# Kernel optimization log

Hardware: AMD Instinct MI355X
Metric: run time of the kernel (lower is better)

The kernel has to match this reference:

```python
import jax, jax.numpy as jnp
import numpy as np

B, T, XD, ZD, H = 1024, 1000, 8, 8, 256


def setup_inputs() -> dict:
    key = jax.random.key(0)
    ks = jax.random.split(key, 10)
    # monotonically increasing time grid, identical per batch element: [B, T, 1]
    t = jnp.broadcast_to(jnp.linspace(0.0, 10.0, T, dtype=jnp.float32)[None, :, None], (B, T, 1))
    x = jax.random.normal(ks[0], (B, T, XD), jnp.float32)
    z = jax.random.normal(ks[1], (B, T, ZD), jnp.float32)
    event_t = jax.random.uniform(ks[2], (B, 1), jnp.float32, 3.0, 7.0)
    z_jump = jax.random.normal(ks[3], (B, ZD), jnp.float32)
    in_dim = 3 * (XD + ZD)

    def lin(k, fan_in, fan_out):
        return jax.random.normal(k, (fan_in, fan_out), jnp.float32) * (1.0 / np.sqrt(fan_in))

    W1 = lin(ks[4], in_dim, H); b1 = jnp.zeros((H,), jnp.float32)
    W2 = lin(ks[5], H, H);     b2 = jnp.zeros((H,), jnp.float32)
    W3 = lin(ks[6], H, H);     b3 = jnp.zeros((H,), jnp.float32)
    W4 = lin(ks[7], H, XD);    b4 = jnp.zeros((XD,), jnp.float32)
    return dict(t=t, x=x, z=z, event_t=event_t, z_jump=z_jump,
                W1=W1, b1=b1, W2=W2, b2=b2, W3=W3, b3=b3, W4=W4, b4=b4)


def reference(t, x, z, event_t, z_jump, W1, b1, W2, b2, W3, b3, W4, b4):
    # all_initial = cat(x[:,0], z[:,0]) : [B, XD+ZD]
    all_initial = jnp.concatenate([x[:, 0], z[:, 0]], axis=-1)

    def de_func(x_cur, z_eff):
        xtzt = jnp.concatenate([x_cur, z_eff], axis=-1)                      # [B, XD+ZD]
        inp = jnp.concatenate([all_initial, xtzt - all_initial, xtzt], -1)   # [B, 3*(XD+ZD)]
        h = jax.nn.elu(inp @ W1 + b1)
        h = jax.nn.elu(h @ W2 + b2)
        h = jax.nn.elu(h @ W3 + b3)
        return h @ W4 + b4                                                   # [B, XD]

    t_seq = jnp.moveaxis(t, 1, 0)   # [T, B, 1]
    z_seq = jnp.moveaxis(z, 1, 0)   # [T, B, ZD]
    dt = t_seq[1:] - t_seq[:-1]     # [T-1, B, 1]

    def step(x_cur, step_in):
        t_i, dt_i, z_i = step_in
        # event: once t passes event_t, exogenous z jumps to z_jump
        z_eff = jnp.where(t_i >= event_t, z_jump, z_i)
        x_next = x_cur + dt_i * de_func(x_cur, z_eff)  # explicit Euler step
        return x_next, x_next

    x0 = x[:, 0]  # initial condition [B, XD]
    _, xs = jax.lax.scan(step, x0, (t_seq[:-1], dt, z_seq[:-1]))
    sol = jnp.concatenate([x0[None], xs], axis=0)  # [T, B, XD]
    return jnp.moveaxis(sol, 0, 1)                 # [B, T, XD]
```

## Files before the change

kernel.cpp:

```cpp
#include <hip/hip_runtime.h>
#include <cstdint>
#include <cstddef>

typedef __bf16 bf16x8 __attribute__((ext_vector_type(8)));
typedef float f32x4 __attribute__((ext_vector_type(4)));

#define HD 256
#define TLEN 1000
#define NSTEP 999
#define BTILE 4

#define W1R_OFF 0
#define W2R_OFF 16384
#define W3R_OFF 81920
#define W4R_OFF 147456
#define WS_ELEMS 151552

__device__ __forceinline__ void wg_barrier() {
  asm volatile("s_waitcnt lgkmcnt(0)\n\ts_barrier" ::: "memory");
}

__global__ void prep_weights(const float* __restrict__ W1, const float* __restrict__ b1,
                             const float* __restrict__ W2, const float* __restrict__ W3,
                             const float* __restrict__ W4, __bf16* __restrict__ ws) {
  int tid = blockIdx.x * blockDim.x + threadIdx.x;
  if (tid >= WS_ELEMS) return;
  float val = 0.0f;
  if (tid < W2R_OFF) {
    int t = tid;
    int j = t & 7, lane = (t >> 3) & 63, tt = (t >> 9) & 1, kb = (t >> 10) & 1, w = (t >> 11) & 7;
    int k = kb * 32 + ((lane >> 4) * 8) + j;
    int n = w * 32 + tt * 16 + (lane & 15);
    if (k < 48) val = W1[k * HD + n];
    else if (k == 48) val = b1[n];
  } else if (tid < W3R_OFF) {
    int t = tid - W2R_OFF;
    int j = t & 7, lane = (t >> 3) & 63, tt = (t >> 9) & 1, kb = (t >> 10) & 7, w = (t >> 13) & 7;
    int k = kb * 32 + ((lane >> 4) * 8) + j;
    int n = w * 32 + tt * 16 + (lane & 15);
    val = W2[k * HD + n];
  } else if (tid < W4R_OFF) {
    int t = tid - W3R_OFF;
    int j = t & 7, lane = (t >> 3) & 63, tt = (t >> 9) & 1, kb = (t >> 10) & 7, w = (t >> 13) & 7;
    int k = kb * 32 + ((lane >> 4) * 8) + j;
    int n = w * 32 + tt * 16 + (lane & 15);
    val = W3[k * HD + n];
  } else {
    int t = tid - W4R_OFF;
    int j = t & 7, lane = (t >> 3) & 63, kb = (t >> 9) & 7;
    int k = kb * 32 + ((lane >> 4) * 8) + j;
    int n = lane & 15;
    val = (n < 8) ? W4[k * 8 + n] : 0.0f;
  }
  ws[tid] = (__bf16)val;
}

__global__ __launch_bounds__(512, 2) void ode_main(
    const float* __restrict__ t_g, const float* __restrict__ x_g,
    const float* __restrict__ z_g, const float* __restrict__ ev_g,
    const float* __restrict__ zj_g, const float* __restrict__ b2_g,
    const float* __restrict__ b3_g, const float* __restrict__ b4_g,
    const __bf16* __restrict__ ws, float* __restrict__ out) {
  __shared__ __align__(16) __bf16 h_a[16 * 264];
  __shared__ __align__(16) __bf16 h_b[16 * 264];
  __shared__ __align__(16) float p4[8 * 16 * 8];
  __shared__ __align__(16) float x_cur[16 * 12];
  __shared__ __align__(16) float z_eff[16 * 12];
  __shared__ __align__(16) float x0s[16 * 12];
  __shared__ __align__(16) float z0s[16 * 12];
  __shared__ __align__(16) float zjs[16 * 12];
  __shared__ float evs[16];

  const int tid  = threadIdx.x;
  const int lane = tid & 63;
  const int wid  = tid >> 6;
  const int bcol = lane & 15;
  const int q    = lane >> 4;
  const int b0   = blockIdx.x * BTILE;
  const bool live = bcol < BTILE;

  if (tid < 128) {
    int m = tid >> 3, d = tid & 7;
    if (m < BTILE) {
      size_t gb = (size_t)(b0 + m);
      float x0 = x_g[gb * (TLEN * 8) + d];
      float z0 = z_g[gb * (TLEN * 8) + d];
      x0s[m * 12 + d] = x0;
      z0s[m * 12 + d] = z0;
      x_cur[m * 12 + d] = x0;
      zjs[m * 12 + d] = zj_g[gb * 8 + d];
      out[gb * (TLEN * 8) + d] = x0;
      if (d == 0) evs[m] = ev_g[gb];
    } else {
      x0s[m * 12 + d] = 0.f;
      z0s[m * 12 + d] = 0.f;
      x_cur[m * 12 + d] = 0.f;
      zjs[m * 12 + d] = 0.f;
      if (d == 0) evs[m] = 0.f;
    }
  }
  __syncthreads();

  if (tid < 128) {
    int m = tid >> 3, d = tid & 7;
    float t0 = t_g[0];
    z_eff[m * 12 + d] = (t0 >= evs[m]) ? zjs[m * 12 + d] : z0s[m * 12 + d];
  }

  const bf16x8* wsv = (const bf16x8*)ws;
  bf16x8 w1f[2][2], w2f[8][2], w3f[8][2];
#pragma unroll
  for (int kb = 0; kb < 2; ++kb)
#pragma unroll
    for (int tt = 0; tt < 2; ++tt)
      w1f[kb][tt] = wsv[(W1R_OFF / 8) + ((wid * 2 + kb) * 2 + tt) * 64 + lane];
#pragma unroll
  for (int kb = 0; kb < 8; ++kb)
#pragma unroll
    for (int tt = 0; tt < 2; ++tt) {
      w2f[kb][tt] = wsv[(W2R_OFF / 8) + ((wid * 8 + kb) * 2 + tt) * 64 + lane];
      w3f[kb][tt] = wsv[(W3R_OFF / 8) + ((wid * 8 + kb) * 2 + tt) * 64 + lane];
    }
  bf16x8 w4f = wsv[(W4R_OFF / 8) + wid * 64 + lane];

  f32x4 b2v[2], b3v[2];
#pragma unroll
  for (int tt = 0; tt < 2; ++tt) {
    int n0 = wid * 32 + tt * 16 + q * 4;
    b2v[tt] = *(const f32x4*)(b2_g + n0);
    b3v[tt] = *(const f32x4*)(b3_g + n0);
  }
  float b4l = (tid < 64) ? b4_g[tid & 7] : 0.0f;

  const int m1 = lane >> 2;
  const int d0 = (lane & 3) * 2;
  float2 zjf = make_float2(0.f, 0.f);
  float ev1 = 0.f;
  const bool zprod = (wid == 2) && (lane < BTILE * 4);
  if (zprod) {
    zjf.x = zjs[m1 * 12 + d0];
    zjf.y = zjs[m1 * 12 + d0 + 1];
    ev1 = evs[m1];
  }

  f32x4 sub0, sub1;
  bf16x8 a0c;
  {
    const float* base = ((q & 1) ? z0s : x0s) + bcol * 12;
    f32x4 r0 = *(const f32x4*)(base);
    f32x4 r1 = *(const f32x4*)(base + 4);
    sub0 = r0; sub1 = r1;
#pragma unroll
    for (int e = 0; e < 4; ++e) { a0c[e] = (__bf16)r0[e]; a0c[e + 4] = (__bf16)r1[e]; }
  }
  bf16x8 zf;
#pragma unroll
  for (int e = 0; e < 8; ++e) zf[e] = (__bf16)0.f;
  bf16x8 k48f = zf;
  k48f[0] = (__bf16)1.0f;

  __syncthreads();

  float tc = t_g[0];

  bf16x8 bfr[8];
#pragma unroll
  for (int kb = 0; kb < 8; ++kb) bfr[kb] = zf;
  bf16x8 h4r = zf;

  auto layer = [&](const __bf16* src, __bf16* dst, const bf16x8 (*wf)[2], const f32x4* bv) {
    const bf16x8* hp = (const bf16x8*)src;
    if (live) {
#pragma unroll
      for (int kb = 0; kb < 8; ++kb) bfr[kb] = hp[bcol * 33 + kb * 4 + q];
    }
#pragma unroll
    for (int tt = 0; tt < 2; ++tt) {
      f32x4 c = bv[tt];
#pragma unroll
      for (int kb = 0; kb < 8; ++kb)
        c = __builtin_amdgcn_mfma_f32_16x16x32_bf16(wf[kb][tt], bfr[kb], c, 0, 0, 0);
      union { __bf16 h4[4]; unsigned long long u; } pk;
#pragma unroll
      for (int e = 0; e < 4; ++e) {
        float v = c[e];
        v = (v > 0.f) ? v : (__expf(v) - 1.0f);
        pk.h4[e] = (__bf16)v;
      }
      if (live)
        *(unsigned long long*)(dst + bcol * 264 + wid * 32 + tt * 16 + q * 4) = pk.u;
    }
  };

#pragma unroll 1
  for (int i = 0; i < NSTEP; ++i) {
    float tn = t_g[i + 1];
    float2 zpre = make_float2(0.f, 0.f);
    if (zprod)
      zpre = *(const float2*)(z_g + ((size_t)(b0 + m1) * TLEN + (i + 1)) * 8 + d0);

    {
      const float* rp = ((q & 1) ? z_eff : x_cur) + bcol * 12;
      f32x4 r0 = *(const f32x4*)(rp);
      f32x4 r1 = *(const f32x4*)(rp + 4);
      bf16x8 f0, f1;
      if (q < 2) {
        f0 = a0c;
#pragma unroll
        for (int e = 0; e < 4; ++e) { f1[e] = (__bf16)r0[e]; f1[e + 4] = (__bf16)r1[e]; }
      } else {
#pragma unroll
        for (int e = 0; e < 4; ++e) {
          f0[e] = (__bf16)(r0[e] - sub0[e]);
          f0[e + 4] = (__bf16)(r1[e] - sub1[e]);
        }
        f1 = (q == 2) ? k48f : zf;
      }
#pragma unroll
      for (int tt = 0; tt < 2; ++tt) {
        f32x4 c = {0.f, 0.f, 0.f, 0.f};
        c = __builtin_amdgcn_mfma_f32_16x16x32_bf16(w1f[0][tt], f0, c, 0, 0, 0);
        c = __builtin_amdgcn_mfma_f32_16x16x32_bf16(w1f[1][tt], f1, c, 0, 0, 0);
        union { __bf16 h4[4]; unsigned long long u; } pk;
#pragma unroll
        for (int e = 0; e < 4; ++e) {
          float v = c[e];
          v = (v > 0.f) ? v : (__expf(v) - 1.0f);
          pk.h4[e] = (__bf16)v;
        }
        if (live)
          *(unsigned long long*)(h_a + bcol * 264 + wid * 32 + tt * 16 + q * 4) = pk.u;
      }
    }
    wg_barrier();
    layer(h_a, h_b, w2f, b2v);
    wg_barrier();
    layer(h_b, h_a, w3f, b3v);

    {
      const bf16x8* hp = (const bf16x8*)h_a;
      if (live) h4r = hp[bcol * 33 + wid * 4 + q];
      f32x4 c = {0.f, 0.f, 0.f, 0.f};
      c = __builtin_amdgcn_mfma_f32_16x16x32_bf16(w4f, h4r, c, 0, 0, 0);
      if (q < 2 && live)
        *(f32x4*)(p4 + wid * 128 + bcol * 8 + q * 4) = c;
    }
    wg_barrier();

    float dt = tn - tc;
    if (tid < 64) {
      int m = tid >> 3, d = tid & 7;
      if (m < BTILE) {
        float s = b4l;
#pragma unroll
        for (int j = 0; j < 8; ++j) s += p4[j * 128 + m * 8 + d];
        float xn = x_cur[m * 12 + d] + dt * s;
        x_cur[m * 12 + d] = xn;
        out[(size_t)(b0 + m) * (TLEN * 8) + (size_t)(i + 1) * 8 + d] = xn;
      }
    } else if (zprod) {
      bool jmp = (tn >= ev1);
      float2 zev = make_float2(jmp ? zjf.x : zpre.x, jmp ? zjf.y : zpre.y);
      *(float2*)(z_eff + m1 * 12 + d0) = zev;
    }
    tc = tn;
    wg_barrier();
  }
}

extern "C" void kernel_launch(void* const* d_in, const int* in_sizes, int n_in,
                              void* d_out, int out_size, void* d_ws, size_t ws_size,
                              hipStream_t stream) {
  const float* t  = (const float*)d_in[0];
  const float* x  = (const float*)d_in[1];
  const float* z  = (const float*)d_in[2];
  const float* ev = (const float*)d_in[3];
  const float* zj = (const float*)d_in[4];
  const float* W1 = (const float*)d_in[5];
  const float* b1 = (const float*)d_in[6];
  const float* W2 = (const float*)d_in[7];
  const float* b2 = (const float*)d_in[8];
  const float* W3 = (const float*)d_in[9];
  const float* b3 = (const float*)d_in[10];
  const float* W4 = (const float*)d_in[11];
  const float* b4 = (const float*)d_in[12];
  __bf16* ws = (__bf16*)d_ws;
  float* out = (float*)d_out;

  prep_weights<<<592, 256, 0, stream>>>(W1, b1, W2, W3, W4, ws);
  ode_main<<<256, 512, 0, stream>>>(t, x, z, ev, zj, b2, b3, b4, ws, out);
}
```

Baseline: 1.671 ms.

## Compute layer-4 redundantly in every wave to drop the partial-sum reduction barrier

Previously each wave computed a slice of the final HxXD product, wrote partials to shared memory, synchronized, and a single wave reduced them and updated x. Now layer 3 writes to a third buffer, and every wave loads the full hidden vector and runs all 8 K-blocks of the output MFMA. Each wave then updates x in registers itself. This replaces the partial-sum barrier with one placed before layer 4, and keeps the state in registers. The cost is redundant MFMA work, more weight registers per wave (w4f grows to 8 fragments), and racy identical writes to x_cur and z_eff from all waves.

```diff
diff --git a/kernel.cpp b/kernel.cpp
--- a/kernel.cpp
+++ b/kernel.cpp
@@ -63,7 +63,7 @@
     const __bf16* __restrict__ ws, float* __restrict__ out) {
   __shared__ __align__(16) __bf16 h_a[16 * 264];
   __shared__ __align__(16) __bf16 h_b[16 * 264];
-  __shared__ __align__(16) float p4[8 * 16 * 8];
+  __shared__ __align__(16) __bf16 h_c[16 * 264];
   __shared__ __align__(16) float x_cur[16 * 12];
   __shared__ __align__(16) float z_eff[16 * 12];
   __shared__ __align__(16) float x0s[16 * 12];
@@ -78,19 +78,20 @@
   const int q    = lane >> 4;
   const int b0   = blockIdx.x * BTILE;
   const bool live = bcol < BTILE;
+  const size_t gb = (size_t)(b0 + (live ? bcol : 0));
 
   if (tid < 128) {
     int m = tid >> 3, d = tid & 7;
     if (m < BTILE) {
-      size_t gb = (size_t)(b0 + m);
-      float x0 = x_g[gb * (TLEN * 8) + d];
-      float z0 = z_g[gb * (TLEN * 8) + d];
+      size_t g = (size_t)(b0 + m);
+      float x0 = x_g[g * (TLEN * 8) + d];
+      float z0 = z_g[g * (TLEN * 8) + d];
       x0s[m * 12 + d] = x0;
       z0s[m * 12 + d] = z0;
       x_cur[m * 12 + d] = x0;
-      zjs[m * 12 + d] = zj_g[gb * 8 + d];
-      out[gb * (TLEN * 8) + d] = x0;
-      if (d == 0) evs[m] = ev_g[gb];
+      zjs[m * 12 + d] = zj_g[g * 8 + d];
+      out[g * (TLEN * 8) + d] = x0;
+      if (d == 0) evs[m] = ev_g[g];
     } else {
       x0s[m * 12 + d] = 0.f;
       z0s[m * 12 + d] = 0.f;
@@ -108,20 +109,21 @@
   }
 
   const bf16x8* wsv = (const bf16x8*)ws;
-  bf16x8 w1f[2][2], w2f[8][2], w3f[8][2];
+  bf16x8 w1f[2][2], w2f[8][2], w3f[8][2], w4f[8];
 #pragma unroll
   for (int kb = 0; kb < 2; ++kb)
 #pragma unroll
     for (int tt = 0; tt < 2; ++tt)
       w1f[kb][tt] = wsv[(W1R_OFF / 8) + ((wid * 2 + kb) * 2 + tt) * 64 + lane];
 #pragma unroll
-  for (int kb = 0; kb < 8; ++kb)
+  for (int kb = 0; kb < 8; ++kb) {
 #pragma unroll
     for (int tt = 0; tt < 2; ++tt) {
       w2f[kb][tt] = wsv[(W2R_OFF / 8) + ((wid * 8 + kb) * 2 + tt) * 64 + lane];
       w3f[kb][tt] = wsv[(W3R_OFF / 8) + ((wid * 8 + kb) * 2 + tt) * 64 + lane];
     }
-  bf16x8 w4f = wsv[(W4R_OFF / 8) + wid * 64 + lane];
+    w4f[kb] = wsv[(W4R_OFF / 8) + kb * 64 + lane];
+  }
 
   f32x4 b2v[2], b3v[2];
 #pragma unroll
@@ -130,14 +132,15 @@
     b2v[tt] = *(const f32x4*)(b2_g + n0);
     b3v[tt] = *(const f32x4*)(b3_g + n0);
   }
-  float b4l = (tid < 64) ? b4_g[tid & 7] : 0.0f;
+  f32x4 b4v = {0.f, 0.f, 0.f, 0.f};
+  if (q < 2) b4v = *(const f32x4*)(b4_g + q * 4);
 
   const int m1 = lane >> 2;
   const int d0 = (lane & 3) * 2;
+  const bool zp = (lane < 16);
   float2 zjf = make_float2(0.f, 0.f);
   float ev1 = 0.f;
-  const bool zprod = (wid == 2) && (lane < BTILE * 4);
-  if (zprod) {
+  if (zp) {
     zjf.x = zjs[m1 * 12 + d0];
     zjf.y = zjs[m1 * 12 + d0 + 1];
     ev1 = evs[m1];
@@ -159,6 +162,9 @@
   bf16x8 k48f = zf;
   k48f[0] = (__bf16)1.0f;
 
+  f32x4 xc4 = {0.f, 0.f, 0.f, 0.f};
+  if (q < 2) xc4 = *(const f32x4*)(x0s + bcol * 12 + q * 4);
+
   __syncthreads();
 
   float tc = t_g[0];
@@ -166,7 +172,6 @@
   bf16x8 bfr[8];
 #pragma unroll
   for (int kb = 0; kb < 8; ++kb) bfr[kb] = zf;
-  bf16x8 h4r = zf;
 
   auto layer = [&](const __bf16* src, __bf16* dst, const bf16x8 (*wf)[2], const f32x4* bv) {
     const bf16x8* hp = (const bf16x8*)src;
@@ -196,7 +201,7 @@
   for (int i = 0; i < NSTEP; ++i) {
     float tn = t_g[i + 1];
     float2 zpre = make_float2(0.f, 0.f);
-    if (zprod)
+    if (zp)
       zpre = *(const float2*)(z_g + ((size_t)(b0 + m1) * TLEN + (i + 1)) * 8 + d0);
 
     {
@@ -235,36 +240,41 @@
     wg_barrier();
     layer(h_a, h_b, w2f, b2v);
     wg_barrier();
-    layer(h_b, h_a, w3f, b3v);
+    layer(h_b, h_c, w3f, b3v);
+    wg_barrier();
 
     {
-      const bf16x8* hp = (const bf16x8*)h_a;
-      if (live) h4r = hp[bcol * 33 + wid * 4 + q];
-      f32x4 c = {0.f, 0.f, 0.f, 0.f};
-      c = __builtin_amdgcn_mfma_f32_16x16x32_bf16(w4f, h4r, c, 0, 0, 0);
-      if (q < 2 && live)
-        *(f32x4*)(p4 + wid * 128 + bcol * 8 + q * 4) = c;
-    }
-    wg_barrier();
-
-    float dt = tn - tc;
-    if (tid < 64) {
-      int m = tid >> 3, d = tid & 7;
-      if (m < BTILE) {
-        float s = b4l;
-#pragma unroll
-        for (int j = 0; j < 8; ++j) s += p4[j * 128 + m * 8 + d];
-        float xn = x_cur[m * 12 + d] + dt * s;
-        x_cur[m * 12 + d] = xn;
-        out[(size_t)(b0 + m) * (TLEN * 8) + (size_t)(i + 1) * 8 + d] = xn;
-      }
-    } else if (zprod) {
-      bool jmp = (tn >= ev1);
-      float2 zev = make_float2(jmp ? zjf.x : zpre.x, jmp ? zjf.y : zpre.y);
-      *(float2*)(z_eff + m1 * 12 + d0) = zev;
+      const bf16x8* hp = (const bf16x8*)h_c;
+      if (live) {
+#pragma unroll
+        for (int kb = 0; kb < 8; ++kb) bfr[kb] = hp[bcol * 33 + kb * 4 + q];
+      }
+      f32x4 c0 = {0.f, 0.f, 0.f, 0.f}, c1 = {0.f, 0.f, 0.f, 0.f};
+#pragma unroll
+      for (int kb = 0; kb < 4; ++kb)
+        c0 = __builtin_amdgcn_mfma_f32_16x16x32_bf16(w4f[kb], bfr[kb], c0, 0, 0, 0);
+#pragma unroll
+      for (int kb = 4; kb < 8; ++kb)
+        c1 = __builtin_amdgcn_mfma_f32_16x16x32_bf16(w4f[kb], bfr[kb], c1, 0, 0, 0);
+      float dt = tn - tc;
+      if (q < 2) {
+        f32x4 xn;
+#pragma unroll
+        for (int e = 0; e < 4; ++e) xn[e] = xc4[e] + dt * (c0[e] + c1[e] + b4v[e]);
+        xc4 = xn;
+        if (live) {
+          *(f32x4*)(x_cur + bcol * 12 + q * 4) = xn;
+          if (wid == 0)
+            *(f32x4*)(out + gb * (TLEN * 8) + (size_t)(i + 1) * 8 + q * 4) = xn;
+        }
+      }
+      if (zp) {
+        bool jmp = (tn >= ev1);
+        float2 zev = make_float2(jmp ? zjf.x : zpre.x, jmp ? zjf.y : zpre.y);
+        *(float2*)(z_eff + m1 * 12 + d0) = zev;
+      }
     }
     tc = tn;
-    wg_barrier();
   }
 }
 
```

Result: slower. 2.786 ms (+66.8%).

## Split each MLP layer across 16 waves, one 16-column tile per wave

Applied to the files above, without the earlier changes.

Doubles the workgroup to 1024 threads so each wave owns a single 16-wide output tile instead of two, halving per-wave MFMA chains and the weight registers each wave holds. Layers 2 and 3 now use two independent accumulators to shorten the dependent MFMA chain. The W4 partial products are split across wave pairs, and the final reduction sums 16 partials. The cost is more waves contending at each barrier and a longer final reduction, and 1024-thread blocks may limit residency per CU.

```diff
diff --git a/kernel.cpp b/kernel.cpp
--- a/kernel.cpp
+++ b/kernel.cpp
@@ -55,7 +55,7 @@
   ws[tid] = (__bf16)val;
 }
 
-__global__ __launch_bounds__(512, 2) void ode_main(
+__global__ __launch_bounds__(1024, 4) void ode_main(
     const float* __restrict__ t_g, const float* __restrict__ x_g,
     const float* __restrict__ z_g, const float* __restrict__ ev_g,
     const float* __restrict__ zj_g, const float* __restrict__ b2_g,
@@ -63,7 +63,7 @@
     const __bf16* __restrict__ ws, float* __restrict__ out) {
   __shared__ __align__(16) __bf16 h_a[16 * 264];
   __shared__ __align__(16) __bf16 h_b[16 * 264];
-  __shared__ __align__(16) float p4[8 * 16 * 8];
+  __shared__ __align__(16) float p4[16 * 128];
   __shared__ __align__(16) float x_cur[16 * 12];
   __shared__ __align__(16) float z_eff[16 * 12];
   __shared__ __align__(16) float x0s[16 * 12];
@@ -74,7 +74,10 @@
   const int tid  = threadIdx.x;
   const int lane = tid & 63;
   const int wid  = tid >> 6;
+  const int pw   = wid >> 1;
+  const int ptt  = wid & 1;
   const int bcol = lane & 15;
+  const int rdcol= bcol & 3;
   const int q    = lane >> 4;
   const int b0   = blockIdx.x * BTILE;
   const bool live = bcol < BTILE;
@@ -82,15 +85,15 @@
   if (tid < 128) {
     int m = tid >> 3, d = tid & 7;
     if (m < BTILE) {
-      size_t gb = (size_t)(b0 + m);
-      float x0 = x_g[gb * (TLEN * 8) + d];
-      float z0 = z_g[gb * (TLEN * 8) + d];
+      size_t g = (size_t)(b0 + m);
+      float x0 = x_g[g * (TLEN * 8) + d];
+      float z0 = z_g[g * (TLEN * 8) + d];
       x0s[m * 12 + d] = x0;
       z0s[m * 12 + d] = z0;
       x_cur[m * 12 + d] = x0;
-      zjs[m * 12 + d] = zj_g[gb * 8 + d];
-      out[gb * (TLEN * 8) + d] = x0;
-      if (d == 0) evs[m] = ev_g[gb];
+      zjs[m * 12 + d] = zj_g[g * 8 + d];
+      out[g * (TLEN * 8) + d] = x0;
+      if (d == 0) evs[m] = ev_g[g];
     } else {
       x0s[m * 12 + d] = 0.f;
       z0s[m * 12 + d] = 0.f;
@@ -108,28 +111,19 @@
   }
 
   const bf16x8* wsv = (const bf16x8*)ws;
-  bf16x8 w1f[2][2], w2f[8][2], w3f[8][2];
+  bf16x8 w1f[2], w2f[8], w3f[8];
 #pragma unroll
   for (int kb = 0; kb < 2; ++kb)
-#pragma unroll
-    for (int tt = 0; tt < 2; ++tt)
-      w1f[kb][tt] = wsv[(W1R_OFF / 8) + ((wid * 2 + kb) * 2 + tt) * 64 + lane];
-#pragma unroll
-  for (int kb = 0; kb < 8; ++kb)
-#pragma unroll
-    for (int tt = 0; tt < 2; ++tt) {
-      w2f[kb][tt] = wsv[(W2R_OFF / 8) + ((wid * 8 + kb) * 2 + tt) * 64 + lane];
-      w3f[kb][tt] = wsv[(W3R_OFF / 8) + ((wid * 8 + kb) * 2 + tt) * 64 + lane];
-    }
-  bf16x8 w4f = wsv[(W4R_OFF / 8) + wid * 64 + lane];
-
-  f32x4 b2v[2], b3v[2];
-#pragma unroll
-  for (int tt = 0; tt < 2; ++tt) {
-    int n0 = wid * 32 + tt * 16 + q * 4;
-    b2v[tt] = *(const f32x4*)(b2_g + n0);
-    b3v[tt] = *(const f32x4*)(b3_g + n0);
-  }
+    w1f[kb] = wsv[(W1R_OFF / 8) + ((pw * 2 + kb) * 2 + ptt) * 64 + lane];
+#pragma unroll
+  for (int kb = 0; kb < 8; ++kb) {
+    w2f[kb] = wsv[(W2R_OFF / 8) + ((pw * 8 + kb) * 2 + ptt) * 64 + lane];
+    w3f[kb] = wsv[(W3R_OFF / 8) + ((pw * 8 + kb) * 2 + ptt) * 64 + lane];
+  }
+  bf16x8 w4f = wsv[(W4R_OFF / 8) + pw * 64 + lane];
+
+  f32x4 b2v = *(const f32x4*)(b2_g + wid * 16 + q * 4);
+  f32x4 b3v = *(const f32x4*)(b3_g + wid * 16 + q * 4);
   float b4l = (tid < 64) ? b4_g[tid & 7] : 0.0f;
 
   const int m1 = lane >> 2;
@@ -143,43 +137,78 @@
     ev1 = evs[m1];
   }
 
-  f32x4 sub0, sub1;
-  bf16x8 a0c;
-  {
-    const float* base = ((q & 1) ? z0s : x0s) + bcol * 12;
-    f32x4 r0 = *(const f32x4*)(base);
-    f32x4 r1 = *(const f32x4*)(base + 4);
-    sub0 = r0; sub1 = r1;
-#pragma unroll
-    for (int e = 0; e < 4; ++e) { a0c[e] = (__bf16)r0[e]; a0c[e + 4] = (__bf16)r1[e]; }
-  }
   bf16x8 zf;
 #pragma unroll
   for (int e = 0; e < 8; ++e) zf[e] = (__bf16)0.f;
-  bf16x8 k48f = zf;
-  k48f[0] = (__bf16)1.0f;
 
   __syncthreads();
 
   float tc = t_g[0];
 
-  bf16x8 bfr[8];
-#pragma unroll
-  for (int kb = 0; kb < 8; ++kb) bfr[kb] = zf;
-  bf16x8 h4r = zf;
-
-  auto layer = [&](const __bf16* src, __bf16* dst, const bf16x8 (*wf)[2], const f32x4* bv) {
+  auto layer = [&](const __bf16* src, __bf16* dst, const bf16x8* wf, f32x4 bv) {
     const bf16x8* hp = (const bf16x8*)src;
-    if (live) {
-#pragma unroll
-      for (int kb = 0; kb < 8; ++kb) bfr[kb] = hp[bcol * 33 + kb * 4 + q];
-    }
-#pragma unroll
-    for (int tt = 0; tt < 2; ++tt) {
-      f32x4 c = bv[tt];
-#pragma unroll
-      for (int kb = 0; kb < 8; ++kb)
-        c = __builtin_amdgcn_mfma_f32_16x16x32_bf16(wf[kb][tt], bfr[kb], c, 0, 0, 0);
+    bf16x8 f0 = hp[rdcol * 33 + 0 * 4 + q];
+    bf16x8 f1 = hp[rdcol * 33 + 1 * 4 + q];
+    bf16x8 f2 = hp[rdcol * 33 + 2 * 4 + q];
+    bf16x8 f3 = hp[rdcol * 33 + 3 * 4 + q];
+    bf16x8 f4 = hp[rdcol * 33 + 4 * 4 + q];
+    bf16x8 f5 = hp[rdcol * 33 + 5 * 4 + q];
+    bf16x8 f6 = hp[rdcol * 33 + 6 * 4 + q];
+    bf16x8 f7 = hp[rdcol * 33 + 7 * 4 + q];
+    f32x4 c0 = bv;
+    f32x4 c1 = {0.f, 0.f, 0.f, 0.f};
+    c0 = __builtin_amdgcn_mfma_f32_16x16x32_bf16(wf[0], f0, c0, 0, 0, 0);
+    c1 = __builtin_amdgcn_mfma_f32_16x16x32_bf16(wf[4], f4, c1, 0, 0, 0);
+    c0 = __builtin_amdgcn_mfma_f32_16x16x32_bf16(wf[1], f1, c0, 0, 0, 0);
+    c1 = __builtin_amdgcn_mfma_f32_16x16x32_bf16(wf[5], f5, c1, 0, 0, 0);
+    c0 = __builtin_amdgcn_mfma_f32_16x16x32_bf16(wf[2], f2, c0, 0, 0, 0);
+    c1 = __builtin_amdgcn_mfma_f32_16x16x32_bf16(wf[6], f6, c1, 0, 0, 0);
+    c0 = __builtin_amdgcn_mfma_f32_16x16x32_bf16(wf[3], f3, c0, 0, 0, 0);
+    c1 = __builtin_amdgcn_mfma_f32_16x16x32_bf16(wf[7], f7, c1, 0, 0, 0);
+    union { __bf16 h4[4]; unsigned long long u; } pk;
+#pragma unroll
+    for (int e = 0; e < 4; ++e) {
+      float v = c0[e] + c1[e];
+      v = (v > 0.f) ? v : (__expf(v) - 1.0f);
+      pk.h4[e] = (__bf16)v;
+    }
+    if (live)
+      *(unsigned long long*)(dst + bcol * 264 + wid * 16 + q * 4) = pk.u;
+  };
+
+#pragma unroll 1
+  for (int i = 0; i < NSTEP; ++i) {
+    float tn = t_g[i + 1];
+    float2 zpre = make_float2(0.f, 0.f);
+    if (zprod)
+      zpre = *(const float2*)(z_g + ((size_t)(b0 + m1) * TLEN + (i + 1)) * 8 + d0);
+
+    {
+      const float* rp = ((q & 1) ? z_eff : x_cur) + bcol * 12;
+      const float* sp = ((q & 1) ? z0s   : x0s  ) + bcol * 12;
+      f32x4 r0 = *(const f32x4*)(rp);
+      f32x4 r1 = *(const f32x4*)(rp + 4);
+      f32x4 s0 = *(const f32x4*)(sp);
+      f32x4 s1 = *(const f32x4*)(sp + 4);
+      bf16x8 f0, f1;
+      if (q < 2) {
+#pragma unroll
+        for (int e = 0; e < 4; ++e) {
+          f0[e] = (__bf16)s0[e]; f0[e + 4] = (__bf16)s1[e];
+          f1[e] = (__bf16)r0[e]; f1[e + 4] = (__bf16)r1[e];
+        }
+      } else {
+#pragma unroll
+        for (int e = 0; e < 4; ++e) {
+          f0[e] = (__bf16)(r0[e] - s0[e]);
+          f0[e + 4] = (__bf16)(r1[e] - s1[e]);
+        }
+        f1 = zf;
+        if (q == 2) f1[0] = (__bf16)1.0f;
+      }
+      f32x4 c = {0.f, 0.f, 0.f, 0.f};
+      c = __builtin_amdgcn_mfma_f32_16x16x32_bf16(w1f[0], f0, c, 0, 0, 0);
+      c = __builtin_amdgcn_mfma_f32_16x16x32_bf16(w1f[1], f1, c, 0, 0, 0);
       union { __bf16 h4[4]; unsigned long long u; } pk;
 #pragma unroll
       for (int e = 0; e < 4; ++e) {
@@ -188,60 +217,19 @@
         pk.h4[e] = (__bf16)v;
       }
       if (live)
-        *(unsigned long long*)(dst + bcol * 264 + wid * 32 + tt * 16 + q * 4) = pk.u;
-    }
-  };
-
-#pragma unroll 1
-  for (int i = 0; i < NSTEP; ++i) {
-    float tn = t_g[i + 1];
-    float2 zpre = make_float2(0.f, 0.f);
-    if (zprod)
-      zpre = *(const float2*)(z_g + ((size_t)(b0 + m1) * TLEN + (i + 1)) * 8 + d0);
+        *(unsigned long long*)(h_a + bcol * 264 + wid * 16 + q * 4) = pk.u;
+    }
+    wg_barrier();
+    layer(h_a, h_b, w2f, b2v);
+    wg_barrier();
+    layer(h_b, h_a, w3f, b3v);
 
     {
-      const float* rp = ((q & 1) ? z_eff : x_cur) + bcol * 12;
-      f32x4 r0 = *(const f32x4*)(rp);
-      f32x4 r1 = *(const f32x4*)(rp + 4);
-      bf16x8 f0, f1;
-      if (q < 2) {
-        f0 = a0c;
-#pragma unroll
-        for (int e = 0; e < 4; ++e) { f1[e] = (__bf16)r0[e]; f1[e + 4] = (__bf16)r1[e]; }
-      } else {
-#pragma unroll
-        for (int e = 0; e < 4; ++e) {
-          f0[e] = (__bf16)(r0[e] - sub0[e]);
-          f0[e + 4] = (__bf16)(r1[e] - sub1[e]);
-        }
-        f1 = (q == 2) ? k48f : zf;
-      }
-#pragma unroll
-      for (int tt = 0; tt < 2; ++tt) {
-        f32x4 c = {0.f, 0.f, 0.f, 0.f};
-        c = __builtin_amdgcn_mfma_f32_16x16x32_bf16(w1f[0][tt], f0, c, 0, 0, 0);
-        c = __builtin_amdgcn_mfma_f32_16x16x32_bf16(w1f[1][tt], f1, c, 0, 0, 0);
-        union { __bf16 h4[4]; unsigned long long u; } pk;
-#pragma unroll
-        for (int e = 0; e < 4; ++e) {
-          float v = c[e];
-          v = (v > 0.f) ? v : (__expf(v) - 1.0f);
-          pk.h4[e] = (__bf16)v;
-        }
-        if (live)
-          *(unsigned long long*)(h_a + bcol * 264 + wid * 32 + tt * 16 + q * 4) = pk.u;
-      }
-    }
-    wg_barrier();
-    layer(h_a, h_b, w2f, b2v);
-    wg_barrier();
-    layer(h_b, h_a, w3f, b3v);
-
-    {
-      const bf16x8* hp = (const bf16x8*)h_a;
-      if (live) h4r = hp[bcol * 33 + wid * 4 + q];
+      bf16x8 h4 = zf;
+      if (live && ((q >> 1) == ptt))
+        h4 = ((const bf16x8*)h_a)[bcol * 33 + pw * 4 + q];
       f32x4 c = {0.f, 0.f, 0.f, 0.f};
-      c = __builtin_amdgcn_mfma_f32_16x16x32_bf16(w4f, h4r, c, 0, 0, 0);
+      c = __builtin_amdgcn_mfma_f32_16x16x32_bf16(w4f, h4, c, 0, 0, 0);
       if (q < 2 && live)
         *(f32x4*)(p4 + wid * 128 + bcol * 8 + q * 4) = c;
     }
@@ -253,7 +241,7 @@
       if (m < BTILE) {
         float s = b4l;
 #pragma unroll
-        for (int j = 0; j < 8; ++j) s += p4[j * 128 + m * 8 + d];
+        for (int j = 0; j < 16; ++j) s += p4[j * 128 + m * 8 + d];
         float xn = x_cur[m * 12 + d] + dt * s;
         x_cur[m * 12 + d] = xn;
         out[(size_t)(b0 + m) * (TLEN * 8) + (size_t)(i + 1) * 8 + d] = xn;
@@ -288,5 +276,5 @@
   float* out = (float*)d_out;
 
   prep_weights<<<592, 256, 0, stream>>>(W1, b1, W2, W3, W4, ws);
-  ode_main<<<256, 512, 0, stream>>>(t, x, z, ev, zj, b2, b3, b4, ws, out);
-}
+  ode_main<<<256, 1024, 0, stream>>>(t, x, z, ev, zj, b2, b3, b4, ws, out);
+}
```

New measurement: 2.252 ms. 34.8% more time.

## Keep Euler state in registers and drop a per-step barrier

Applied to the files above, without the earlier changes.

Each wave now keeps the ODE state x and the effective z in registers. Every wave redundantly reduces the layer-4 partials from LDS and applies the Euler update, with wave shuffles assembling the layer-1 input. This removes the dedicated update phase and one workgroup barrier per time step, and the z and t loads for the next step are issued early. It also splits the layer-2/3 MFMA accumulation into two independent chains to shorten dependency latency, at the cost of redundant reduction work in every wave and a slightly different floating-point summation order.

```diff
diff --git a/kernel.cpp b/kernel.cpp
--- a/kernel.cpp
+++ b/kernel.cpp
@@ -63,13 +63,9 @@
     const __bf16* __restrict__ ws, float* __restrict__ out) {
   __shared__ __align__(16) __bf16 h_a[16 * 264];
   __shared__ __align__(16) __bf16 h_b[16 * 264];
-  __shared__ __align__(16) float p4[8 * 16 * 8];
-  __shared__ __align__(16) float x_cur[16 * 12];
-  __shared__ __align__(16) float z_eff[16 * 12];
+  __shared__ __align__(16) float p4[8 * 128];
   __shared__ __align__(16) float x0s[16 * 12];
   __shared__ __align__(16) float z0s[16 * 12];
-  __shared__ __align__(16) float zjs[16 * 12];
-  __shared__ float evs[16];
 
   const int tid  = threadIdx.x;
   const int lane = tid & 63;
@@ -78,34 +74,21 @@
   const int q    = lane >> 4;
   const int b0   = blockIdx.x * BTILE;
   const bool live = bcol < BTILE;
-
-  if (tid < 128) {
-    int m = tid >> 3, d = tid & 7;
-    if (m < BTILE) {
-      size_t gb = (size_t)(b0 + m);
-      float x0 = x_g[gb * (TLEN * 8) + d];
-      float z0 = z_g[gb * (TLEN * 8) + d];
-      x0s[m * 12 + d] = x0;
-      z0s[m * 12 + d] = z0;
-      x_cur[m * 12 + d] = x0;
-      zjs[m * 12 + d] = zj_g[gb * 8 + d];
-      out[gb * (TLEN * 8) + d] = x0;
-      if (d == 0) evs[m] = ev_g[gb];
-    } else {
-      x0s[m * 12 + d] = 0.f;
-      z0s[m * 12 + d] = 0.f;
-      x_cur[m * 12 + d] = 0.f;
-      zjs[m * 12 + d] = 0.f;
-      if (d == 0) evs[m] = 0.f;
-    }
-  }
+  const size_t gb = (size_t)(b0 + (live ? bcol : 0));
+
+  if (tid < 192) {
+    int m = tid / 12, d = tid % 12;
+    float xv = 0.f, zv = 0.f;
+    if (m < BTILE && d < 8) {
+      size_t g = (size_t)(b0 + m);
+      xv = x_g[g * (TLEN * 8) + d];
+      zv = z_g[g * (TLEN * 8) + d];
+    }
+    x0s[m * 12 + d] = xv;
+    z0s[m * 12 + d] = zv;
+  }
+  if (tid < 512) { p4[tid] = 0.f; if (tid < 512) { int t2 = tid + 512; if (t2 < 1024) p4[t2] = 0.f; } }
   __syncthreads();
-
-  if (tid < 128) {
-    int m = tid >> 3, d = tid & 7;
-    float t0 = t_g[0];
-    z_eff[m * 12 + d] = (t0 >= evs[m]) ? zjs[m * 12 + d] : z0s[m * 12 + d];
-  }
 
   const bf16x8* wsv = (const bf16x8*)ws;
   bf16x8 w1f[2][2], w2f[8][2], w3f[8][2];
@@ -130,18 +113,8 @@
     b2v[tt] = *(const f32x4*)(b2_g + n0);
     b3v[tt] = *(const f32x4*)(b3_g + n0);
   }
-  float b4l = (tid < 64) ? b4_g[tid & 7] : 0.0f;
-
-  const int m1 = lane >> 2;
-  const int d0 = (lane & 3) * 2;
-  float2 zjf = make_float2(0.f, 0.f);
-  float ev1 = 0.f;
-  const bool zprod = (wid == 2) && (lane < BTILE * 4);
-  if (zprod) {
-    zjf.x = zjs[m1 * 12 + d0];
-    zjf.y = zjs[m1 * 12 + d0 + 1];
-    ev1 = evs[m1];
-  }
+  f32x4 b4v = {0.f, 0.f, 0.f, 0.f};
+  if (q < 2) b4v = *(const f32x4*)(b4_g + q * 4);
 
   f32x4 sub0, sub1;
   bf16x8 a0c;
@@ -159,9 +132,19 @@
   bf16x8 k48f = zf;
   k48f[0] = (__bf16)1.0f;
 
-  __syncthreads();
-
-  float tc = t_g[0];
+  f32x4 x4 = {0.f, 0.f, 0.f, 0.f};
+  if (q < 2) x4 = *(const f32x4*)(x0s + bcol * 12 + q * 4);
+
+  float ev1 = 0.f;
+  f32x4 zjA = {0.f, 0.f, 0.f, 0.f}, zjB = {0.f, 0.f, 0.f, 0.f};
+  f32x4 zpA = {0.f, 0.f, 0.f, 0.f}, zpB = {0.f, 0.f, 0.f, 0.f};
+  if ((q & 1) && live) {
+    ev1 = ev_g[gb];
+    zjA = *(const f32x4*)(zj_g + gb * 8);
+    zjB = *(const f32x4*)(zj_g + gb * 8 + 4);
+    zpA = *(const f32x4*)(z_g + gb * (TLEN * 8));
+    zpB = *(const f32x4*)(z_g + gb * (TLEN * 8) + 4);
+  }
 
   bf16x8 bfr[8];
 #pragma unroll
@@ -176,10 +159,104 @@
     }
 #pragma unroll
     for (int tt = 0; tt < 2; ++tt) {
-      f32x4 c = bv[tt];
-#pragma unroll
-      for (int kb = 0; kb < 8; ++kb)
-        c = __builtin_amdgcn_mfma_f32_16x16x32_bf16(wf[kb][tt], bfr[kb], c, 0, 0, 0);
+      f32x4 c0 = bv[tt];
+      f32x4 c1 = {0.f, 0.f, 0.f, 0.f};
+#pragma unroll
+      for (int kb = 0; kb < 4; ++kb)
+        c0 = __builtin_amdgcn_mfma_f32_16x16x32_bf16(wf[kb][tt], bfr[kb], c0, 0, 0, 0);
+#pragma unroll
+      for (int kb = 4; kb < 8; ++kb)
+        c1 = __builtin_amdgcn_mfma_f32_16x16x32_bf16(wf[kb][tt], bfr[kb], c1, 0, 0, 0);
+      union { __bf16 h4[4]; unsigned long long u; } pk;
+#pragma unroll
+      for (int e = 0; e < 4; ++e) {
+        float v = c0[e] + c1[e];
+        v = (v > 0.f) ? v : (__expf(v) - 1.0f);
+        pk.h4[e] = (__bf16)v;
+      }
+      if (live)
+        *(unsigned long long*)(dst + bcol * 264 + wid * 32 + tt * 16 + q * 4) = pk.u;
+    }
+  };
+
+  float tc = t_g[0];
+  float tn_hold = tc;
+  __syncthreads();
+
+#pragma unroll 1
+  for (int i = 0; i <= NSTEP; ++i) {
+    float tn = tn_hold;
+    float dt = tn - tc;
+    tc = tn;
+    if (q < 2 && live) {
+      const float* pp = p4 + bcol * 8 + q * 4;
+      f32x4 a0 = *(const f32x4*)(pp + 0 * 128);
+      f32x4 a1 = *(const f32x4*)(pp + 1 * 128);
+      f32x4 a2 = *(const f32x4*)(pp + 2 * 128);
+      f32x4 a3 = *(const f32x4*)(pp + 3 * 128);
+      f32x4 a4 = *(const f32x4*)(pp + 4 * 128);
+      f32x4 a5 = *(const f32x4*)(pp + 5 * 128);
+      f32x4 a6 = *(const f32x4*)(pp + 6 * 128);
+      f32x4 a7 = *(const f32x4*)(pp + 7 * 128);
+      f32x4 s = ((a0 + a1) + (a2 + a3)) + ((a4 + a5) + (a6 + a7));
+#pragma unroll
+      for (int e = 0; e < 4; ++e) x4[e] += dt * (s[e] + b4v[e]);
+      if (wid == 0)
+        *(f32x4*)(out + gb * (TLEN * 8) + (size_t)i * 8 + q * 4) = x4;
+    }
+    if (i == NSTEP) break;
+
+    f32x4 o4, lo, hi, xlo, xhi;
+#pragma unroll
+    for (int e = 0; e < 4; ++e) o4[e] = __shfl_xor(x4[e], 16);
+#pragma unroll
+    for (int e = 0; e < 4; ++e) {
+      lo[e] = (q & 1) ? o4[e] : x4[e];
+      hi[e] = (q & 1) ? x4[e] : o4[e];
+    }
+#pragma unroll
+    for (int e = 0; e < 4; ++e) {
+      float l2 = __shfl_xor(lo[e], 32);
+      float h2 = __shfl_xor(hi[e], 32);
+      xlo[e] = (q >= 2) ? l2 : lo[e];
+      xhi[e] = (q >= 2) ? h2 : hi[e];
+    }
+    bool jmp = (tn >= ev1);
+    f32x4 zelo, zehi;
+#pragma unroll
+    for (int e = 0; e < 4; ++e) {
+      zelo[e] = jmp ? zjA[e] : zpA[e];
+      zehi[e] = jmp ? zjB[e] : zpB[e];
+    }
+    bf16x8 f0, f1;
+    if (q == 0) {
+      f0 = a0c;
+#pragma unroll
+      for (int e = 0; e < 4; ++e) { f1[e] = (__bf16)xlo[e]; f1[e + 4] = (__bf16)xhi[e]; }
+    } else if (q == 1) {
+      f0 = a0c;
+#pragma unroll
+      for (int e = 0; e < 4; ++e) { f1[e] = (__bf16)zelo[e]; f1[e + 4] = (__bf16)zehi[e]; }
+    } else if (q == 2) {
+#pragma unroll
+      for (int e = 0; e < 4; ++e) {
+        f0[e] = (__bf16)(xlo[e] - sub0[e]);
+        f0[e + 4] = (__bf16)(xhi[e] - sub1[e]);
+      }
+      f1 = k48f;
+    } else {
+#pragma unroll
+      for (int e = 0; e < 4; ++e) {
+        f0[e] = (__bf16)(zelo[e] - sub0[e]);
+        f0[e + 4] = (__bf16)(zehi[e] - sub1[e]);
+      }
+      f1 = zf;
+    }
+#pragma unroll
+    for (int tt = 0; tt < 2; ++tt) {
+      f32x4 c = {0.f, 0.f, 0.f, 0.f};
+      c = __builtin_amdgcn_mfma_f32_16x16x32_bf16(w1f[0][tt], f0, c, 0, 0, 0);
+      c = __builtin_amdgcn_mfma_f32_16x16x32_bf16(w1f[1][tt], f1, c, 0, 0, 0);
       union { __bf16 h4[4]; unsigned long long u; } pk;
 #pragma unroll
       for (int e = 0; e < 4; ++e) {
@@ -188,82 +265,26 @@
         pk.h4[e] = (__bf16)v;
       }
       if (live)
-        *(unsigned long long*)(dst + bcol * 264 + wid * 32 + tt * 16 + q * 4) = pk.u;
-    }
-  };
-
-#pragma unroll 1
-  for (int i = 0; i < NSTEP; ++i) {
-    float tn = t_g[i + 1];
-    float2 zpre = make_float2(0.f, 0.f);
-    if (zprod)
-      zpre = *(const float2*)(z_g + ((size_t)(b0 + m1) * TLEN + (i + 1)) * 8 + d0);
-
-    {
-      const float* rp = ((q & 1) ? z_eff : x_cur) + bcol * 12;
-      f32x4 r0 = *(const f32x4*)(rp);
-      f32x4 r1 = *(const f32x4*)(rp + 4);
-      bf16x8 f0, f1;
-      if (q < 2) {
-        f0 = a0c;
-#pragma unroll
-        for (int e = 0; e < 4; ++e) { f1[e] = (__bf16)r0[e]; f1[e + 4] = (__bf16)r1[e]; }
-      } else {
-#pragma unroll
-        for (int e = 0; e < 4; ++e) {
-          f0[e] = (__bf16)(r0[e] - sub0[e]);
-          f0[e + 4] = (__bf16)(r1[e] - sub1[e]);
-        }
-        f1 = (q == 2) ? k48f : zf;
-      }
-#pragma unroll
-      for (int tt = 0; tt < 2; ++tt) {
-        f32x4 c = {0.f, 0.f, 0.f, 0.f};
-        c = __builtin_amdgcn_mfma_f32_16x16x32_bf16(w1f[0][tt], f0, c, 0, 0, 0);
-        c = __builtin_amdgcn_mfma_f32_16x16x32_bf16(w1f[1][tt], f1, c, 0, 0, 0);
-        union { __bf16 h4[4]; unsigned long long u; } pk;
-#pragma unroll
-        for (int e = 0; e < 4; ++e) {
-          float v = c[e];
-          v = (v > 0.f) ? v : (__expf(v) - 1.0f);
-          pk.h4[e] = (__bf16)v;
-        }
-        if (live)
-          *(unsigned long long*)(h_a + bcol * 264 + wid * 32 + tt * 16 + q * 4) = pk.u;
-      }
+        *(unsigned long long*)(h_a + bcol * 264 + wid * 32 + tt * 16 + q * 4) = pk.u;
     }
     wg_barrier();
+
+    if ((q & 1) && live) {
+      zpA = *(const f32x4*)(z_g + gb * (TLEN * 8) + (size_t)(i + 1) * 8);
+      zpB = *(const f32x4*)(z_g + gb * (TLEN * 8) + (size_t)(i + 1) * 8 + 4);
+    }
+    tn_hold = t_g[i + 1];
     layer(h_a, h_b, w2f, b2v);
     wg_barrier();
+
     layer(h_b, h_a, w3f, b3v);
-
     {
-      const bf16x8* hp = (const bf16x8*)h_a;
-      if (live) h4r = hp[bcol * 33 + wid * 4 + q];
+      if (live) h4r = ((const bf16x8*)h_a)[bcol * 33 + wid * 4 + q];
       f32x4 c = {0.f, 0.f, 0.f, 0.f};
       c = __builtin_amdgcn_mfma_f32_16x16x32_bf16(w4f, h4r, c, 0, 0, 0);
       if (q < 2 && live)
         *(f32x4*)(p4 + wid * 128 + bcol * 8 + q * 4) = c;
     }
-    wg_barrier();
-
-    float dt = tn - tc;
-    if (tid < 64) {
-      int m = tid >> 3, d = tid & 7;
-      if (m < BTILE) {
-        float s = b4l;
-#pragma unroll
-        for (int j = 0; j < 8; ++j) s += p4[j * 128 + m * 8 + d];
-        float xn = x_cur[m * 12 + d] + dt * s;
-        x_cur[m * 12 + d] = xn;
-        out[(size_t)(b0 + m) * (TLEN * 8) + (size_t)(i + 1) * 8 + d] = xn;
-      }
-    } else if (zprod) {
-      bool jmp = (tn >= ev1);
-      float2 zev = make_float2(jmp ? zjf.x : zpre.x, jmp ? zjf.y : zpre.y);
-      *(float2*)(z_eff + m1 * 12 + d0) = zev;
-    }
-    tc = tn;
     wg_barrier();
   }
 }
```

Result: slower. 3.523 ms (+110.8%).
